# Optimization experiments

Hardware: AMD Instinct MI355X
Metric: run time of the kernel (lower is better)

## Reference

```python
import jax, jax.numpy as jnp
import numpy as np
from jax import lax

SEQ, BATCH, IN_W = 2048, 64, 256
STREAM_W = 1024
OUT_W = 64


def _range(num, lo, hi):
    return np.arange(num, dtype=np.float64) / float(num - 1) * (hi - lo) + lo


def _sin_buffers(width):
    # Faithful to ResSin: tau = 2*pi, w_min = -2*tau, w_max = 2*tau
    tau = 2.0 * np.pi
    w_max = 2.0 * tau
    l_num = width // 2
    r_num = width - l_num
    inner = np.concatenate([
        _range(l_num, -w_max, -1.0 / l_num),
        _range(r_num, 1.0 / r_num, w_max),
    ])
    outer = np.concatenate([
        _range(l_num, -1.0, -w_max),
        _range(r_num, w_max, 1.0),
    ]) / inner
    return inner.astype(np.float32), outer.astype(np.float32)


def setup_inputs() -> dict:
    key = jax.random.key(0)
    ks = jax.random.split(key, 7)
    W = STREAM_W
    inner, outer = _sin_buffers(W)
    scale = 1.0 / np.sqrt(W)
    return {
        "input": jax.random.normal(ks[0], (SEQ, BATCH, IN_W), dtype=jnp.float32),
        "initial_stream": jax.random.normal(ks[1], (W,), dtype=jnp.float32) * 0.02,
        "w1": jax.random.normal(ks[2], (W, W), dtype=jnp.float32) * scale,
        "b1": jax.random.normal(ks[3], (W,), dtype=jnp.float32) * 0.01,
        "w2": jax.random.normal(ks[4], (W, W), dtype=jnp.float32) * scale,
        "b2": jax.random.normal(ks[5], (W,), dtype=jnp.float32) * 0.01,
        "bendiness": jax.random.normal(ks[6], (W,), dtype=jnp.float32) * 0.1,
        "inner_weight": jnp.asarray(inner),
        "outer_weight": jnp.asarray(outer),
    }


def reference(input, initial_stream, w1, b1, w2, b2, bendiness, inner_weight, outer_weight):
    S, B, I = input.shape
    W = initial_stream.shape[0]
    pad = W - I
    stream0 = jnp.broadcast_to(initial_stream, (B, W))

    def step(stream, elem):
        # Add: pad input element up to stream width and add residually
        s = stream + jnp.pad(elem, ((0, 0), (0, pad)))
        # ResLinear fc1: addmm(bias, x, weight.T)
        h = s @ w1.T + b1
        # ResSin: x + bendiness * outer * sin(x * inner)
        h = h + bendiness * outer_weight * jnp.sin(h * inner_weight)
        # ResLinear fc2
        s = h @ w2.T + b2
        return s, None

    final, _ = lax.scan(step, stream0, input)
    # seq_indices = -1 (default): every batch element takes the last stream
    outputs = final[:, :OUT_W]
    return outputs, final
```

## Files before the change

kernel.cpp:

```cpp
#include <hip/hip_runtime.h>
#include <math.h>


#define WDIM 1024
#define SEQ_N 2048
#define LDS8 81920
#define LDSL 163840

__device__ __forceinline__ double gload(const double* p) {
  unsigned long long v = __hip_atomic_load((const unsigned long long*)p,
                                           __ATOMIC_RELAXED, __HIP_MEMORY_SCOPE_AGENT);
  return __builtin_bit_cast(double, v);
}
__device__ __forceinline__ void gstore(double* p, double d) {
  __hip_atomic_store((unsigned long long*)p, __builtin_bit_cast(unsigned long long, d),
                     __ATOMIC_RELAXED, __HIP_MEMORY_SCOPE_AGENT);
}

__device__ __forceinline__ void gbar_acq(unsigned* barR, unsigned target, int leaf,
                                         unsigned perleaf, unsigned leaves) {
  __syncthreads();
  if (threadIdx.x == 0) {
    __builtin_amdgcn_fence(__ATOMIC_RELEASE, "agent");
    unsigned old = __hip_atomic_fetch_add(&barR[32 + leaf * 16], 1u, __ATOMIC_RELAXED,
                                          __HIP_MEMORY_SCOPE_AGENT);
    if (old + 1u == target * perleaf) {
      unsigned r = __hip_atomic_fetch_add(&barR[16], 1u, __ATOMIC_RELAXED,
                                          __HIP_MEMORY_SCOPE_AGENT);
      if (r + 1u == target * leaves)
        __hip_atomic_store(&barR[0], target, __ATOMIC_RELAXED, __HIP_MEMORY_SCOPE_AGENT);
    }
    while (__hip_atomic_load(&barR[0], __ATOMIC_RELAXED, __HIP_MEMORY_SCOPE_AGENT) < target)
      __builtin_amdgcn_s_sleep(2);
  }
  __syncthreads();
  __builtin_amdgcn_fence(__ATOMIC_ACQUIRE, "agent");
}

__device__ __forceinline__ void gbarL(unsigned* barR, unsigned target, int leaf,
                                      unsigned perleaf, unsigned leaves) {
  __syncthreads();
  if (threadIdx.x == 0) {
    __builtin_amdgcn_fence(__ATOMIC_RELEASE, "agent");
    unsigned old = __hip_atomic_fetch_add(&barR[32 + leaf * 16], 1u, __ATOMIC_RELAXED,
                                          __HIP_MEMORY_SCOPE_AGENT);
    if (old + 1u == target * perleaf) {
      unsigned r = __hip_atomic_fetch_add(&barR[16], 1u, __ATOMIC_RELAXED,
                                          __HIP_MEMORY_SCOPE_AGENT);
      if (r + 1u == target * leaves)
        __hip_atomic_store(&barR[0], target, __ATOMIC_RELAXED, __HIP_MEMORY_SCOPE_AGENT);
    }
    while (__hip_atomic_load(&barR[0], __ATOMIC_RELAXED, __HIP_MEMORY_SCOPE_AGENT) < target)
      __builtin_amdgcn_s_sleep(2);
  }
  __syncthreads();
}

__global__ __launch_bounds__(256) void k_gemm_wt(const float* __restrict__ A,
                                                 const float* __restrict__ B,
                                                 double* __restrict__ Wcd) {
  __shared__ float As[32][68];
  __shared__ float Bs[32][68];
  const int tid = threadIdx.x;
  const int tx = tid & 15, ty = tid >> 4;
  const int bx = blockIdx.x, by = blockIdx.y;
  double acc[4][4] = {};
  for (int j0 = 0; j0 < WDIM; j0 += 32) {
    for (int l = tid; l < 64 * 32; l += 256) {
      int r = l >> 5, c = l & 31;
      As[c][r] = A[(by * 64 + r) * WDIM + j0 + c];
    }
    for (int l = tid; l < 32 * 64; l += 256) {
      int r = l >> 6, c = l & 63;
      Bs[r][c] = B[(j0 + r) * WDIM + bx * 64 + c];
    }
    __syncthreads();
#pragma unroll 8
    for (int kk = 0; kk < 32; ++kk) {
      float a[4], bb[4];
      *(float4*)a  = *(const float4*)&As[kk][ty * 4];
      *(float4*)bb = *(const float4*)&Bs[kk][tx * 4];
#pragma unroll
      for (int i = 0; i < 4; ++i)
#pragma unroll
        for (int j = 0; j < 4; ++j) acc[i][j] += (double)a[i] * (double)bb[j];
    }
    __syncthreads();
  }
#pragma unroll
  for (int i = 0; i < 4; ++i)
#pragma unroll
    for (int j = 0; j < 4; ++j)
      Wcd[(size_t)(by * 64 + ty * 4 + i) * WDIM + bx * 64 + tx * 4 + j] = acc[i][j];
}

__global__ __launch_bounds__(256) void k_bias(const float* __restrict__ W1,
                                              const float* __restrict__ b1,
                                              const float* __restrict__ b2,
                                              const float* __restrict__ s0,
                                              double* __restrict__ b1c,
                                              double* __restrict__ c0, unsigned* bar) {
  if (blockIdx.x < 16) bar[blockIdx.x * 256 + threadIdx.x] = 0u;
  int wave = threadIdx.x >> 6;
  int lane = threadIdx.x & 63;
  int n = blockIdx.x * 4 + wave;
  const float* row = W1 + (size_t)n * WDIM;
  double a1 = 0.0, a2 = 0.0;
  for (int k = lane; k < WDIM; k += 64) {
    double w = (double)row[k];
    a1 += (double)b2[k] * w;
    a2 += (double)s0[k] * w;
  }
#pragma unroll
  for (int off = 32; off; off >>= 1) {
    a1 += __shfl_down(a1, off, 64);
    a2 += __shfl_down(a2, off, 64);
  }
  if (lane == 0) { b1c[n] = (double)b1[n] + a1; c0[n] = (double)b1[n] + a2; }
}

__global__ __launch_bounds__(256, 2) void k_main8(
    const float* __restrict__ x, const double* __restrict__ Wcd,
    const float* __restrict__ W1, const double* __restrict__ b1c,
    const double* __restrict__ c0, const float* __restrict__ W2,
    const float* __restrict__ b2, const float* __restrict__ bend,
    const float* __restrict__ inner, const float* __restrict__ outer,
    double* vA, double* vB, float* __restrict__ out, unsigned* bar) {
  extern __shared__ double2 tile[];
  double* red = (double*)(tile + 4096);
  const int tid = threadIdx.x;
  const int ks = tid & 31;
  const int bg = (tid >> 5) & 1;
  const int ng = tid >> 6;
  const int nt = blockIdx.x & 63, g = blockIdx.x >> 6;
  const int leaf = nt >> 3;
  unsigned* barG = bar + g * 512;

  if (tid < 128) gstore(&vA[blockIdx.x * 128 + tid], 0.0);

  const double* wrow[4];
  const float* w1row[4];
  const float* w2row[4];
#pragma unroll
  for (int jn = 0; jn < 4; ++jn) {
    int n = nt * 16 + ng * 4 + jn;
    wrow[jn]  = Wcd + (size_t)n * WDIM;
    w1row[jn] = W1 + (size_t)n * WDIM;
    w2row[jn] = W2 + (size_t)n * WDIM;
  }

  const int n_red = nt * 16 + (tid & 15);
  const int b_red = g * 8 + ((tid >> 4) & 7);
  const double bo   = (double)bend[n_red] * (double)outer[n_red];
  const double inw  = (double)inner[n_red];
  const double b1cr = b1c[n_red];
  const double c0r  = c0[n_red];
  const int oswz = (ng * 4) & 15;

  unsigned gent = 0;
  double* vin = vA;
  double* vout = vB;
  gbar_acq(barG, ++gent, leaf, 8u, 8u);

  for (int t = 0; t < SEQ_N; ++t) {
    float2 xv[4][4], wv[4][4];
#pragma unroll
    for (int i = 0; i < 4; ++i) {
      int c2 = i * 32 + ks;
#pragma unroll
      for (int r = 0; r < 4; ++r)
        xv[r][i] = ((const float2*)(x + ((size_t)t * 64 + g * 8 + bg * 4 + r) * 256))[c2];
#pragma unroll
      for (int jn = 0; jn < 4; ++jn)
        wv[jn][i] = ((const float2*)w1row[jn])[c2];
    }
    double2 vld[16];
#pragma unroll
    for (int j = 0; j < 16; ++j) {
      int idx = j * 256 + tid;
      int r = idx >> 9, c2 = idx & 511;
      vld[j] = *(const double2*)(vin + (size_t)(g * 8 + r) * WDIM + c2 * 2);
    }
    double accx[4][4], accy[4][4];
#pragma unroll
    for (int ib = 0; ib < 4; ++ib)
#pragma unroll
      for (int jn = 0; jn < 4; ++jn) { accx[ib][jn] = 0.0; accy[ib][jn] = 0.0; }
#pragma unroll
    for (int i = 0; i < 4; ++i)
#pragma unroll
      for (int jn = 0; jn < 4; ++jn) {
        double wx = (double)wv[jn][i].x, wy = (double)wv[jn][i].y;
        accx[0][jn] += (double)xv[0][i].x * wx; accy[0][jn] += (double)xv[0][i].y * wy;
        accx[1][jn] += (double)xv[1][i].x * wx; accy[1][jn] += (double)xv[1][i].y * wy;
        accx[2][jn] += (double)xv[2][i].x * wx; accy[2][jn] += (double)xv[2][i].y * wy;
        accx[3][jn] += (double)xv[3][i].x * wx; accy[3][jn] += (double)xv[3][i].y * wy;
      }
#pragma unroll
    for (int j = 0; j < 16; ++j)
      tile[j * 256 + tid] = vld[j];
    __syncthreads();
#pragma unroll 4
    for (int i = 0; i < 16; ++i) {
      int c2 = i * 32 + ks;
      double2 v0 = tile[(bg * 4 + 0) * 512 + c2];
      double2 v1 = tile[(bg * 4 + 1) * 512 + c2];
      double2 v2 = tile[(bg * 4 + 2) * 512 + c2];
      double2 v3 = tile[(bg * 4 + 3) * 512 + c2];
#pragma unroll
      for (int jn = 0; jn < 4; ++jn) {
        double2 w = ((const double2*)wrow[jn])[c2];
        accx[0][jn] += v0.x * w.x; accy[0][jn] += v0.y * w.y;
        accx[1][jn] += v1.x * w.x; accy[1][jn] += v1.y * w.y;
        accx[2][jn] += v2.x * w.x; accy[2][jn] += v2.y * w.y;
        accx[3][jn] += v3.x * w.x; accy[3][jn] += v3.y * w.y;
      }
    }
#pragma unroll
    for (int ib = 0; ib < 4; ++ib)
#pragma unroll
      for (int jn = 0; jn < 4; ++jn) {
        double p = accx[ib][jn] + accy[ib][jn];
        p += __shfl_xor(p, 16, 64);
        if (ks < 16) {
          int o = (bg * 4 + ib) * 16 + ng * 4 + jn;
          red[o * 16 + (ks ^ ((oswz + jn) & 15))] = p;
        }
      }
    __syncthreads();
    if (tid < 128) {
      double s = 0.0;
      const int oc = tid & 15;
#pragma unroll
      for (int slc = 0; slc < 16; ++slc)
        s += red[tid * 16 + (slc ^ oc)];
      double u = s + (t == 0 ? c0r : b1cr);
      double gv = u + bo * sin(u * inw);
      gstore(&vout[(size_t)b_red * WDIM + n_red], gv);
    }
    gbar_acq(barG, ++gent, leaf, 8u, 8u);
    double* tmp = vin; vin = vout; vout = tmp;
  }

  {
    double2 vld[16];
#pragma unroll
    for (int j = 0; j < 16; ++j) {
      int idx = j * 256 + tid;
      int r = idx >> 9, c2 = idx & 511;
      vld[j] = *(const double2*)(vin + (size_t)(g * 8 + r) * WDIM + c2 * 2);
    }
#pragma unroll
    for (int j = 0; j < 16; ++j)
      tile[j * 256 + tid] = vld[j];
    __syncthreads();
    double accx[4][4], accy[4][4];
#pragma unroll
    for (int ib = 0; ib < 4; ++ib)
#pragma unroll
      for (int jn = 0; jn < 4; ++jn) { accx[ib][jn] = 0.0; accy[ib][jn] = 0.0; }
#pragma unroll 4
    for (int i = 0; i < 16; ++i) {
      int c2 = i * 32 + ks;
      double2 v0 = tile[(bg * 4 + 0) * 512 + c2];
      double2 v1 = tile[(bg * 4 + 1) * 512 + c2];
      double2 v2 = tile[(bg * 4 + 2) * 512 + c2];
      double2 v3 = tile[(bg * 4 + 3) * 512 + c2];
#pragma unroll
      for (int jn = 0; jn < 4; ++jn) {
        float2 wf = ((const float2*)w2row[jn])[c2];
        double wx = (double)wf.x, wy = (double)wf.y;
        accx[0][jn] += v0.x * wx; accy[0][jn] += v0.y * wy;
        accx[1][jn] += v1.x * wx; accy[1][jn] += v1.y * wy;
        accx[2][jn] += v2.x * wx; accy[2][jn] += v2.y * wy;
        accx[3][jn] += v3.x * wx; accy[3][jn] += v3.y * wy;
      }
    }
#pragma unroll
    for (int ib = 0; ib < 4; ++ib)
#pragma unroll
      for (int jn = 0; jn < 4; ++jn) {
        double p = accx[ib][jn] + accy[ib][jn];
        p += __shfl_xor(p, 16, 64);
        if (ks < 16) {
          int o = (bg * 4 + ib) * 16 + ng * 4 + jn;
          red[o * 16 + (ks ^ ((oswz + jn) & 15))] = p;
        }
      }
    __syncthreads();
    if (tid < 128) {
      double s = 0.0;
      const int oc = tid & 15;
#pragma unroll
      for (int slc = 0; slc < 16; ++slc)
        s += red[tid * 16 + (slc ^ oc)];
      double sv = s + (double)b2[n_red];
      out[4096 + (size_t)b_red * WDIM + n_red] = (float)sv;
      if (n_red < 64) out[(size_t)b_red * 64 + n_red] = (float)sv;
    }
  }
}

__global__ __launch_bounds__(512, 2) void k_main(
    const float* __restrict__ x, const double* __restrict__ Wcd,
    const float* __restrict__ W1, const double* __restrict__ b1c,
    const double* __restrict__ c0, const float* __restrict__ W2,
    const float* __restrict__ b2, const float* __restrict__ bend,
    const float* __restrict__ inner, const float* __restrict__ outer,
    double* vA, double* vB, float* __restrict__ out, unsigned* bar) {
  extern __shared__ double2 tile[];
  double* red = (double*)(tile + 8192);
  const int tid = threadIdx.x;
  const int ks = tid & 31;
  const int bg = (tid >> 5) & 3;
  const int ng = (tid >> 7) & 3;
  const int nt = blockIdx.x & 63, g = blockIdx.x >> 6;
  const int leaf = blockIdx.x >> 4;

  if (tid < 256) vA[blockIdx.x * 256 + tid] = 0.0;

  const double* wrow[4];
  const float* w1row[4];
  const float* w2row[4];
#pragma unroll
  for (int jn = 0; jn < 4; ++jn) {
    int n = nt * 16 + ng * 4 + jn;
    wrow[jn]  = Wcd + (size_t)n * WDIM;
    w1row[jn] = W1 + (size_t)n * WDIM;
    w2row[jn] = W2 + (size_t)n * WDIM;
  }
  const int n_red = nt * 16 + (tid & 15);
  const int b_red = g * 16 + ((tid >> 4) & 15);
  const double bo   = (double)bend[n_red] * (double)outer[n_red];
  const double inw  = (double)inner[n_red];
  const double b1cr = b1c[n_red];
  const double c0r  = c0[n_red];
  const int oswz = (ng * 4) & 15;

  unsigned gent = 0;
  double* vin = vA;
  double* vout = vB;
  gbarL(bar, ++gent, leaf, 16u, 16u);

  for (int t = 0; t < SEQ_N; ++t) {
    float2 xv[4][4], wv[4][4];
#pragma unroll
    for (int i = 0; i < 4; ++i) {
      int c2 = i * 32 + ks;
#pragma unroll
      for (int r = 0; r < 4; ++r)
        xv[r][i] = ((const float2*)(x + ((size_t)t * 64 + g * 16 + bg * 4 + r) * 256))[c2];
#pragma unroll
      for (int jn = 0; jn < 4; ++jn)
        wv[jn][i] = ((const float2*)w1row[jn])[c2];
    }
    double va[16], vb[16];
    {
      const double* srcb = vin + (size_t)(g * 16) * WDIM + tid * 2;
#pragma unroll
      for (int j = 0; j < 16; ++j) {
        va[j] = gload(srcb + (size_t)j * WDIM);
        vb[j] = gload(srcb + (size_t)j * WDIM + 1);
      }
    }
    double accx[4][4], accy[4][4];
#pragma unroll
    for (int ib = 0; ib < 4; ++ib)
#pragma unroll
      for (int jn = 0; jn < 4; ++jn) { accx[ib][jn] = 0.0; accy[ib][jn] = 0.0; }
#pragma unroll
    for (int i = 0; i < 4; ++i)
#pragma unroll
      for (int jn = 0; jn < 4; ++jn) {
        double wx = (double)wv[jn][i].x, wy = (double)wv[jn][i].y;
        accx[0][jn] += (double)xv[0][i].x * wx; accy[0][jn] += (double)xv[0][i].y * wy;
        accx[1][jn] += (double)xv[1][i].x * wx; accy[1][jn] += (double)xv[1][i].y * wy;
        accx[2][jn] += (double)xv[2][i].x * wx; accy[2][jn] += (double)xv[2][i].y * wy;
        accx[3][jn] += (double)xv[3][i].x * wx; accy[3][jn] += (double)xv[3][i].y * wy;
      }
#pragma unroll
    for (int j = 0; j < 16; ++j)
      tile[j * 512 + tid] = make_double2(va[j], vb[j]);
    __syncthreads();
#pragma unroll 4
    for (int i = 0; i < 16; ++i) {
      int c2 = i * 32 + ks;
      double2 v0 = tile[(bg * 4 + 0) * 512 + c2];
      double2 v1 = tile[(bg * 4 + 1) * 512 + c2];
      double2 v2 = tile[(bg * 4 + 2) * 512 + c2];
      double2 v3 = tile[(bg * 4 + 3) * 512 + c2];
#pragma unroll
      for (int jn = 0; jn < 4; ++jn) {
        double2 w = ((const double2*)wrow[jn])[c2];
        accx[0][jn] += v0.x * w.x; accy[0][jn] += v0.y * w.y;
        accx[1][jn] += v1.x * w.x; accy[1][jn] += v1.y * w.y;
        accx[2][jn] += v2.x * w.x; accy[2][jn] += v2.y * w.y;
        accx[3][jn] += v3.x * w.x; accy[3][jn] += v3.y * w.y;
      }
    }
#pragma unroll
    for (int ib = 0; ib < 4; ++ib)
#pragma unroll
      for (int jn = 0; jn < 4; ++jn) {
        double p = accx[ib][jn] + accy[ib][jn];
        p += __shfl_xor(p, 16, 64);
        if (ks < 16) {
          int o = (bg * 4 + ib) * 16 + ng * 4 + jn;
          red[o * 16 + (ks ^ ((oswz + jn) & 15))] = p;
        }
      }
    __syncthreads();
    if (tid < 256) {
      double s = 0.0;
      const int oc = tid & 15;
#pragma unroll
      for (int slc = 0; slc < 16; ++slc)
        s += red[tid * 16 + (slc ^ oc)];
      double u = s + (t == 0 ? c0r : b1cr);
      double gv = u + bo * sin(u * inw);
      gstore(&vout[(size_t)b_red * WDIM + n_red], gv);
    }
    gbarL(bar, ++gent, leaf, 16u, 16u);
    double* tmp = vin; vin = vout; vout = tmp;
  }
  {
    double va[16], vb[16];
    {
      const double* srcb = vin + (size_t)(g * 16) * WDIM + tid * 2;
#pragma unroll
      for (int j = 0; j < 16; ++j) {
        va[j] = gload(srcb + (size_t)j * WDIM);
        vb[j] = gload(srcb + (size_t)j * WDIM + 1);
      }
    }
#pragma unroll
    for (int j = 0; j < 16; ++j)
      tile[j * 512 + tid] = make_double2(va[j], vb[j]);
    __syncthreads();
    double accx[4][4], accy[4][4];
#pragma unroll
    for (int ib = 0; ib < 4; ++ib)
#pragma unroll
      for (int jn = 0; jn < 4; ++jn) { accx[ib][jn] = 0.0; accy[ib][jn] = 0.0; }
#pragma unroll 4
    for (int i = 0; i < 16; ++i) {
      int c2 = i * 32 + ks;
      double2 v0 = tile[(bg * 4 + 0) * 512 + c2];
      double2 v1 = tile[(bg * 4 + 1) * 512 + c2];
      double2 v2 = tile[(bg * 4 + 2) * 512 + c2];
      double2 v3 = tile[(bg * 4 + 3) * 512 + c2];
#pragma unroll
      for (int jn = 0; jn < 4; ++jn) {
        float2 wf = ((const float2*)w2row[jn])[c2];
        double wx = (double)wf.x, wy = (double)wf.y;
        accx[0][jn] += v0.x * wx; accy[0][jn] += v0.y * wy;
        accx[1][jn] += v1.x * wx; accy[1][jn] += v1.y * wy;
        accx[2][jn] += v2.x * wx; accy[2][jn] += v2.y * wy;
        accx[3][jn] += v3.x * wx; accy[3][jn] += v3.y * wy;
      }
    }
#pragma unroll
    for (int ib = 0; ib < 4; ++ib)
#pragma unroll
      for (int jn = 0; jn < 4; ++jn) {
        double p = accx[ib][jn] + accy[ib][jn];
        p += __shfl_xor(p, 16, 64);
        if (ks < 16) {
          int o = (bg * 4 + ib) * 16 + ng * 4 + jn;
          red[o * 16 + (ks ^ ((oswz + jn) & 15))] = p;
        }
      }
    __syncthreads();
    if (tid < 256) {
      double s = 0.0;
      const int oc = tid & 15;
#pragma unroll
      for (int slc = 0; slc < 16; ++slc)
        s += red[tid * 16 + (slc ^ oc)];
      double sv = s + (double)b2[n_red];
      out[4096 + (size_t)b_red * WDIM + n_red] = (float)sv;
      if (n_red < 64) out[(size_t)b_red * 64 + n_red] = (float)sv;
    }
  }
}

extern "C" void kernel_launch(void* const* d_in, const int* in_sizes, int n_in,
                              void* d_out, int out_size, void* d_ws, size_t ws_size,
                              hipStream_t stream) {
  const float* x    = (const float*)d_in[0];
  const float* s0   = (const float*)d_in[1];
  const float* W1   = (const float*)d_in[2];
  const float* b1   = (const float*)d_in[3];
  const float* W2   = (const float*)d_in[4];
  const float* b2   = (const float*)d_in[5];
  const float* bend = (const float*)d_in[6];
  const float* inner= (const float*)d_in[7];
  const float* outer= (const float*)d_in[8];
  double* ws = (double*)d_ws;

  double* Wcd = ws;
  double* b1c = ws + 1048576;
  double* c0  = ws + 1049600;
  double* vA  = ws + 1050624;
  double* vB  = ws + 1116160;
  unsigned* bar = (unsigned*)(ws + 1181696);
  float* out = (float*)d_out;

  k_gemm_wt<<<dim3(16, 16), 256, 0, stream>>>(W1, W2, Wcd);
  k_bias<<<256, 256, 0, stream>>>(W1, b1, b2, s0, b1c, c0, bar);

  static bool attr_done = false;
  if (!attr_done) {
    hipFuncSetAttribute((const void*)k_main8, hipFuncAttributeMaxDynamicSharedMemorySize, LDS8);
    hipFuncSetAttribute((const void*)k_main,  hipFuncAttributeMaxDynamicSharedMemorySize, LDSL);
    attr_done = true;
  }

  void* args[] = { (void*)&x, (void*)&Wcd, (void*)&W1, (void*)&b1c, (void*)&c0,
                   (void*)&W2, (void*)&b2, (void*)&bend, (void*)&inner, (void*)&outer,
                   (void*)&vA, (void*)&vB, (void*)&out, (void*)&bar };

  int maxB8 = 0;
  hipError_t q8 = hipOccupancyMaxActiveBlocksPerMultiprocessor(&maxB8, k_main8, 256, LDS8);
  if (q8 == hipSuccess && maxB8 >= 2) {
    if (hipLaunchCooperativeKernel((void*)k_main8, dim3(512), dim3(256), args,
                                   LDS8, stream) != hipSuccess)
      k_main8<<<dim3(512), dim3(256), LDS8, stream>>>(
          x, Wcd, W1, b1c, c0, W2, b2, bend, inner, outer, vA, vB, out, bar);
  } else {
    if (hipLaunchCooperativeKernel((void*)k_main, dim3(256), dim3(512), args,
                                   LDSL, stream) != hipSuccess)
      k_main<<<dim3(256), dim3(512), LDSL, stream>>>(
          x, Wcd, W1, b1c, c0, W2, b2, bend, inner, outer, vA, vB, out, bar);
  }
}
```

Baseline: 36.44 ms.

## Share per-XCC state-vector loads through scratch and drop global barrier fences

The 8-batch, 256-thread persistent kernel is replaced by a 512-thread, 16-batch variant. Blocks on the same XCC and batch group now split the loading of the previous state rows, write them to a per-XCC scratch buffer, meet at a local flag barrier, invalidate the cache, and read the shared copy. The aim is to cut redundant global/L2 traffic for the recurrent state. The global barrier loses its release/acquire fences and uses s_waitcnt instead, which lowers barrier latency. The cost is an extra intra-XCC barrier every step and reliance on weaker memory-ordering assumptions.

```diff
diff --git a/kernel.cpp b/kernel.cpp
--- a/kernel.cpp
+++ b/kernel.cpp
@@ -4,8 +4,8 @@
 
 #define WDIM 1024
 #define SEQ_N 2048
-#define LDS8 81920
-#define LDSL 163840
+#define NB 256
+#define LDS_BYTES 163840
 
 __device__ __forceinline__ double gload(const double* p) {
   unsigned long long v = __hip_atomic_load((const unsigned long long*)p,
@@ -17,40 +17,37 @@
                      __ATOMIC_RELAXED, __HIP_MEMORY_SCOPE_AGENT);
 }
 
-__device__ __forceinline__ void gbar_acq(unsigned* barR, unsigned target, int leaf,
-                                         unsigned perleaf, unsigned leaves) {
+__device__ __forceinline__ void gbarNF(unsigned* bar, unsigned target, int leaf) {
+  asm volatile("s_waitcnt vmcnt(0)" ::: "memory");
+  __syncthreads();
+  if (threadIdx.x == 0) {
+    unsigned old = __hip_atomic_fetch_add(&bar[32 + leaf * 16], 1u, __ATOMIC_RELAXED,
+                                          __HIP_MEMORY_SCOPE_AGENT);
+    if (old + 1u == target * 16u) {
+      unsigned r = __hip_atomic_fetch_add(&bar[16], 1u, __ATOMIC_RELAXED,
+                                          __HIP_MEMORY_SCOPE_AGENT);
+      if (r + 1u == target * 16u)
+        __hip_atomic_store(&bar[0], target, __ATOMIC_RELAXED, __HIP_MEMORY_SCOPE_AGENT);
+    }
+    while (__hip_atomic_load(&bar[0], __ATOMIC_RELAXED, __HIP_MEMORY_SCOPE_AGENT) < target)
+      __builtin_amdgcn_s_sleep(2);
+  }
+  __syncthreads();
+}
+
+__device__ __forceinline__ void gbarF(unsigned* bar, unsigned target, int leaf) {
   __syncthreads();
   if (threadIdx.x == 0) {
     __builtin_amdgcn_fence(__ATOMIC_RELEASE, "agent");
-    unsigned old = __hip_atomic_fetch_add(&barR[32 + leaf * 16], 1u, __ATOMIC_RELAXED,
+    unsigned old = __hip_atomic_fetch_add(&bar[32 + leaf * 16], 1u, __ATOMIC_RELAXED,
                                           __HIP_MEMORY_SCOPE_AGENT);
-    if (old + 1u == target * perleaf) {
-      unsigned r = __hip_atomic_fetch_add(&barR[16], 1u, __ATOMIC_RELAXED,
+    if (old + 1u == target * 16u) {
+      unsigned r = __hip_atomic_fetch_add(&bar[16], 1u, __ATOMIC_RELAXED,
                                           __HIP_MEMORY_SCOPE_AGENT);
-      if (r + 1u == target * leaves)
-        __hip_atomic_store(&barR[0], target, __ATOMIC_RELAXED, __HIP_MEMORY_SCOPE_AGENT);
-    }
-    while (__hip_atomic_load(&barR[0], __ATOMIC_RELAXED, __HIP_MEMORY_SCOPE_AGENT) < target)
-      __builtin_amdgcn_s_sleep(2);
-  }
-  __syncthreads();
-  __builtin_amdgcn_fence(__ATOMIC_ACQUIRE, "agent");
-}
-
-__device__ __forceinline__ void gbarL(unsigned* barR, unsigned target, int leaf,
-                                      unsigned perleaf, unsigned leaves) {
-  __syncthreads();
-  if (threadIdx.x == 0) {
-    __builtin_amdgcn_fence(__ATOMIC_RELEASE, "agent");
-    unsigned old = __hip_atomic_fetch_add(&barR[32 + leaf * 16], 1u, __ATOMIC_RELAXED,
-                                          __HIP_MEMORY_SCOPE_AGENT);
-    if (old + 1u == target * perleaf) {
-      unsigned r = __hip_atomic_fetch_add(&barR[16], 1u, __ATOMIC_RELAXED,
-                                          __HIP_MEMORY_SCOPE_AGENT);
-      if (r + 1u == target * leaves)
-        __hip_atomic_store(&barR[0], target, __ATOMIC_RELAXED, __HIP_MEMORY_SCOPE_AGENT);
-    }
-    while (__hip_atomic_load(&barR[0], __ATOMIC_RELAXED, __HIP_MEMORY_SCOPE_AGENT) < target)
+      if (r + 1u == target * 16u)
+        __hip_atomic_store(&bar[0], target, __ATOMIC_RELAXED, __HIP_MEMORY_SCOPE_AGENT);
+    }
+    while (__hip_atomic_load(&bar[0], __ATOMIC_RELAXED, __HIP_MEMORY_SCOPE_AGENT) < target)
       __builtin_amdgcn_s_sleep(2);
   }
   __syncthreads();
@@ -119,24 +116,39 @@
   if (lane == 0) { b1c[n] = (double)b1[n] + a1; c0[n] = (double)b1[n] + a2; }
 }
 
-__global__ __launch_bounds__(256, 2) void k_main8(
+__global__ __launch_bounds__(512, 2) void k_mainX(
     const float* __restrict__ x, const double* __restrict__ Wcd,
     const float* __restrict__ W1, const double* __restrict__ b1c,
     const double* __restrict__ c0, const float* __restrict__ W2,
     const float* __restrict__ b2, const float* __restrict__ bend,
     const float* __restrict__ inner, const float* __restrict__ outer,
-    double* vA, double* vB, float* __restrict__ out, unsigned* bar) {
+    double* vA, double* vB, double* scratch, float* __restrict__ out,
+    unsigned* bar) {
   extern __shared__ double2 tile[];
-  double* red = (double*)(tile + 4096);
+  double* red = (double*)(tile + 8192);
+  unsigned* meta = (unsigned*)red;
   const int tid = threadIdx.x;
   const int ks = tid & 31;
-  const int bg = (tid >> 5) & 1;
-  const int ng = tid >> 6;
+  const int bg = (tid >> 5) & 3;
+  const int ng = (tid >> 7) & 3;
   const int nt = blockIdx.x & 63, g = blockIdx.x >> 6;
-  const int leaf = nt >> 3;
-  unsigned* barG = bar + g * 512;
-
-  if (tid < 128) gstore(&vA[blockIdx.x * 128 + tid], 0.0);
+  const int leaf = blockIdx.x >> 4;
+
+  if (tid == 0) {
+    unsigned xcc;
+    asm volatile("s_getreg_b32 %0, hwreg(HW_REG_XCC_ID)" : "=s"(xcc));
+    unsigned pr = (xcc & 7u) * 4u + (unsigned)g;
+    unsigned rk = __hip_atomic_fetch_add(&bar[1536 + pr], 1u, __ATOMIC_RELAXED,
+                                         __HIP_MEMORY_SCOPE_AGENT);
+    meta[0] = pr; meta[1] = rk;
+  }
+  __syncthreads();
+  const unsigned pair = meta[0];
+  const unsigned rank = meta[1];
+  unsigned* xflag = bar + 512 + pair * 16;
+  double* scr0 = scratch + (size_t)pair * 2 * 16384;
+
+  if (tid < 256) gstore(&vA[blockIdx.x * 256 + tid], 0.0);
 
   const double* wrow[4];
   const float* w1row[4];
@@ -150,7 +162,7 @@
   }
 
   const int n_red = nt * 16 + (tid & 15);
-  const int b_red = g * 8 + ((tid >> 4) & 7);
+  const int b_red = g * 16 + ((tid >> 4) & 15);
   const double bo   = (double)bend[n_red] * (double)outer[n_red];
   const double inw  = (double)inner[n_red];
   const double b1cr = b1c[n_red];
@@ -160,26 +172,38 @@
   unsigned gent = 0;
   double* vin = vA;
   double* vout = vB;
-  gbar_acq(barG, ++gent, leaf, 8u, 8u);
+  gbarNF(bar, ++gent, leaf);
+
+  if (tid == 0)
+    meta[2] = __hip_atomic_load(&bar[1536 + pair], __ATOMIC_RELAXED,
+                                __HIP_MEMORY_SCOPE_AGENT);
+  __syncthreads();
+  const unsigned nPair = meta[2];
 
   for (int t = 0; t < SEQ_N; ++t) {
+    double* scr = scr0 + (size_t)(t & 1) * 16384;
     float2 xv[4][4], wv[4][4];
 #pragma unroll
     for (int i = 0; i < 4; ++i) {
       int c2 = i * 32 + ks;
 #pragma unroll
       for (int r = 0; r < 4; ++r)
-        xv[r][i] = ((const float2*)(x + ((size_t)t * 64 + g * 8 + bg * 4 + r) * 256))[c2];
+        xv[r][i] = ((const float2*)(x + ((size_t)t * 64 + g * 16 + bg * 4 + r) * 256))[c2];
 #pragma unroll
       for (int jn = 0; jn < 4; ++jn)
         wv[jn][i] = ((const float2*)w1row[jn])[c2];
     }
-    double2 vld[16];
-#pragma unroll
-    for (int j = 0; j < 16; ++j) {
-      int idx = j * 256 + tid;
-      int r = idx >> 9, c2 = idx & 511;
-      vld[j] = *(const double2*)(vin + (size_t)(g * 8 + r) * WDIM + c2 * 2);
+    __builtin_amdgcn_sched_barrier(0);
+    const int r0 = (int)rank, r1 = (int)(rank + nPair);
+    const bool h0 = r0 < 16, h1 = r1 < 16;
+    double a0 = 0, a1 = 0, b0 = 0, b1 = 0;
+    if (h0) {
+      const double* s = vin + (size_t)(g * 16 + r0) * WDIM + tid * 2;
+      a0 = gload(s); a1 = gload(s + 1);
+    }
+    if (h1) {
+      const double* s = vin + (size_t)(g * 16 + r1) * WDIM + tid * 2;
+      b0 = gload(s); b1 = gload(s + 1);
     }
     double accx[4][4], accy[4][4];
 #pragma unroll
@@ -196,10 +220,32 @@
         accx[2][jn] += (double)xv[2][i].x * wx; accy[2][jn] += (double)xv[2][i].y * wy;
         accx[3][jn] += (double)xv[3][i].x * wx; accy[3][jn] += (double)xv[3][i].y * wy;
       }
+    if (h0) *(double2*)(scr + (size_t)r0 * WDIM + tid * 2) = make_double2(a0, a1);
+    if (h1) *(double2*)(scr + (size_t)r1 * WDIM + tid * 2) = make_double2(b0, b1);
+    for (int r = (int)(rank + 2 * nPair); r < 16; r += (int)nPair) {
+      const double* s = vin + (size_t)(g * 16 + r) * WDIM + tid * 2;
+      double d0 = gload(s), d1 = gload(s + 1);
+      *(double2*)(scr + (size_t)r * WDIM + tid * 2) = make_double2(d0, d1);
+    }
+    __syncthreads();
+    if (tid == 0) {
+      __hip_atomic_fetch_add(&xflag[0], 1u, __ATOMIC_RELAXED, __HIP_MEMORY_SCOPE_AGENT);
+      unsigned tgt = (unsigned)(t + 1) * nPair;
+      while (__hip_atomic_load(&xflag[0], __ATOMIC_RELAXED, __HIP_MEMORY_SCOPE_AGENT) < tgt)
+        __builtin_amdgcn_s_sleep(1);
+    }
+    __syncthreads();
+    asm volatile("buffer_inv" ::: "memory");
+
+    double2 vld[16];
 #pragma unroll
     for (int j = 0; j < 16; ++j)
-      tile[j * 256 + tid] = vld[j];
-    __syncthreads();
+      vld[j] = *(const double2*)(scr + (size_t)j * WDIM + tid * 2);
+#pragma unroll
+    for (int j = 0; j < 16; ++j)
+      tile[j * 512 + tid] = vld[j];
+    __syncthreads();
+
 #pragma unroll 4
     for (int i = 0; i < 16; ++i) {
       int c2 = i * 32 + ks;
@@ -228,7 +274,7 @@
         }
       }
     __syncthreads();
-    if (tid < 128) {
+    if (tid < 256) {
       double s = 0.0;
       const int oc = tid & 15;
 #pragma unroll
@@ -238,21 +284,23 @@
       double gv = u + bo * sin(u * inw);
       gstore(&vout[(size_t)b_red * WDIM + n_red], gv);
     }
-    gbar_acq(barG, ++gent, leaf, 8u, 8u);
+    gbarNF(bar, ++gent, leaf);
     double* tmp = vin; vin = vout; vout = tmp;
   }
 
   {
-    double2 vld[16];
-#pragma unroll
-    for (int j = 0; j < 16; ++j) {
-      int idx = j * 256 + tid;
-      int r = idx >> 9, c2 = idx & 511;
-      vld[j] = *(const double2*)(vin + (size_t)(g * 8 + r) * WDIM + c2 * 2);
+    double va[16], vb[16];
+    {
+      const double* srcb = vin + (size_t)(g * 16) * WDIM + tid * 2;
+#pragma unroll
+      for (int j = 0; j < 16; ++j) {
+        va[j] = gload(srcb + (size_t)j * WDIM);
+        vb[j] = gload(srcb + (size_t)j * WDIM + 1);
+      }
     }
 #pragma unroll
     for (int j = 0; j < 16; ++j)
-      tile[j * 256 + tid] = vld[j];
+      tile[j * 512 + tid] = make_double2(va[j], vb[j]);
     __syncthreads();
     double accx[4][4], accy[4][4];
 #pragma unroll
@@ -288,7 +336,7 @@
         }
       }
     __syncthreads();
-    if (tid < 128) {
+    if (tid < 256) {
       double s = 0.0;
       const int oc = tid & 15;
 #pragma unroll
@@ -340,7 +388,7 @@
   unsigned gent = 0;
   double* vin = vA;
   double* vout = vB;
-  gbarL(bar, ++gent, leaf, 16u, 16u);
+  gbarF(bar, ++gent, leaf);
 
   for (int t = 0; t < SEQ_N; ++t) {
     float2 xv[4][4], wv[4][4];
@@ -420,7 +468,7 @@
       double gv = u + bo * sin(u * inw);
       gstore(&vout[(size_t)b_red * WDIM + n_red], gv);
     }
-    gbarL(bar, ++gent, leaf, 16u, 16u);
+    gbarF(bar, ++gent, leaf);
     double* tmp = vin; vin = vout; vout = tmp;
   }
   {
@@ -504,6 +552,8 @@
   double* vA  = ws + 1050624;
   double* vB  = ws + 1116160;
   unsigned* bar = (unsigned*)(ws + 1181696);
+  double* scratch = ws + 1183744;
+  const size_t ws_needed = (size_t)(1183744 + 1048576) * 8;
   float* out = (float*)d_out;
 
   k_gemm_wt<<<dim3(16, 16), 256, 0, stream>>>(W1, W2, Wcd);
@@ -511,26 +561,26 @@
 
   static bool attr_done = false;
   if (!attr_done) {
-    hipFuncSetAttribute((const void*)k_main8, hipFuncAttributeMaxDynamicSharedMemorySize, LDS8);
-    hipFuncSetAttribute((const void*)k_main,  hipFuncAttributeMaxDynamicSharedMemorySize, LDSL);
+    hipFuncSetAttribute((const void*)k_mainX, hipFuncAttributeMaxDynamicSharedMemorySize, LDS_BYTES);
+    hipFuncSetAttribute((const void*)k_main,  hipFuncAttributeMaxDynamicSharedMemorySize, LDS_BYTES);
     attr_done = true;
   }
 
-  void* args[] = { (void*)&x, (void*)&Wcd, (void*)&W1, (void*)&b1c, (void*)&c0,
-                   (void*)&W2, (void*)&b2, (void*)&bend, (void*)&inner, (void*)&outer,
-                   (void*)&vA, (void*)&vB, (void*)&out, (void*)&bar };
-
-  int maxB8 = 0;
-  hipError_t q8 = hipOccupancyMaxActiveBlocksPerMultiprocessor(&maxB8, k_main8, 256, LDS8);
-  if (q8 == hipSuccess && maxB8 >= 2) {
-    if (hipLaunchCooperativeKernel((void*)k_main8, dim3(512), dim3(256), args,
-                                   LDS8, stream) != hipSuccess)
-      k_main8<<<dim3(512), dim3(256), LDS8, stream>>>(
+  if (ws_size >= ws_needed) {
+    void* args[] = { (void*)&x, (void*)&Wcd, (void*)&W1, (void*)&b1c, (void*)&c0,
+                     (void*)&W2, (void*)&b2, (void*)&bend, (void*)&inner, (void*)&outer,
+                     (void*)&vA, (void*)&vB, (void*)&scratch, (void*)&out, (void*)&bar };
+    if (hipLaunchCooperativeKernel((void*)k_mainX, dim3(NB), dim3(512), args,
+                                   LDS_BYTES, stream) != hipSuccess)
+      k_mainX<<<dim3(NB), dim3(512), LDS_BYTES, stream>>>(
+          x, Wcd, W1, b1c, c0, W2, b2, bend, inner, outer, vA, vB, scratch, out, bar);
+  } else {
+    void* args[] = { (void*)&x, (void*)&Wcd, (void*)&W1, (void*)&b1c, (void*)&c0,
+                     (void*)&W2, (void*)&b2, (void*)&bend, (void*)&inner, (void*)&outer,
+                     (void*)&vA, (void*)&vB, (void*)&out, (void*)&bar };
+    if (hipLaunchCooperativeKernel((void*)k_main, dim3(NB), dim3(512), args,
+                                   LDS_BYTES, stream) != hipSuccess)
+      k_main<<<dim3(NB), dim3(512), LDS_BYTES, stream>>>(
           x, Wcd, W1, b1c, c0, W2, b2, bend, inner, outer, vA, vB, out, bar);
-  } else {
-    if (hipLaunchCooperativeKernel((void*)k_main, dim3(256), dim3(512), args,
-                                   LDSL, stream) != hipSuccess)
-      k_main<<<dim3(256), dim3(512), LDSL, stream>>>(
-          x, Wcd, W1, b1c, c0, W2, b2, bend, inner, outer, vA, vB, out, bar);
-  }
-}
+  }
+}
```

After: 40.70 ms. 1.12x slower.
